# Optimization experiments

Hardware: AMD Instinct MI355X
Metric: run time of the kernel (lower is better)

## Reference

```python
import jax, jax.numpy as jnp
import numpy as np

B, N, D = 16, 1024, 768
H = 12
HD = D // H
HID = 4 * D
EPS = 1e-6


def _layernorm(x, g, b):
    mu = jnp.mean(x, axis=-1, keepdims=True)
    var = jnp.mean(jnp.square(x - mu), axis=-1, keepdims=True)
    return (x - mu) * jax.lax.rsqrt(var + EPS) * g + b


def setup_inputs() -> dict:
    key = jax.random.key(0)
    ks = jax.random.split(key, 8)
    s_d = 1.0 / np.sqrt(D)
    s_h = 1.0 / np.sqrt(HID)
    return {
        "x": jax.random.normal(ks[0], (B, N, D), dtype=jnp.float32),
        "qkv_w": jax.random.uniform(ks[1], (3 * D, D), jnp.float32, -s_d, s_d),
        "proj_w": jax.random.uniform(ks[2], (D, D), jnp.float32, -s_d, s_d),
        "proj_b": jax.random.uniform(ks[3], (D,), jnp.float32, -s_d, s_d),
        "fc1_w": jax.random.uniform(ks[4], (HID, D), jnp.float32, -s_d, s_d),
        "fc1_b": jax.random.uniform(ks[5], (HID,), jnp.float32, -s_d, s_d),
        "fc2_w": jax.random.uniform(ks[6], (D, HID), jnp.float32, -s_h, s_h),
        "fc2_b": jax.random.uniform(ks[7], (D,), jnp.float32, -s_h, s_h),
        "norm1_g": jnp.ones((D,), jnp.float32),
        "norm1_b": jnp.zeros((D,), jnp.float32),
        "norm2_g": jnp.ones((D,), jnp.float32),
        "norm2_b": jnp.zeros((D,), jnp.float32),
    }


def _attention(x, qkv_w, proj_w, proj_b):
    b, n, _ = x.shape
    qkv = x @ qkv_w.T                                  # [b,n,3D] (no bias: qkv_bias=False)
    qkv = qkv.reshape(b, n, 3, H, HD)
    q, k, v = (jnp.transpose(qkv[:, :, i], (0, 2, 1, 3)) for i in range(3))  # [b,h,n,hd]
    scale = HD ** (-0.5)
    dots = jnp.einsum("bhid,bhjd->bhij", q, k) * scale
    attn = jax.nn.softmax(dots, axis=-1)
    out = jnp.einsum("bhij,bhjd->bhid", attn, v)
    out = jnp.transpose(out, (0, 2, 1, 3)).reshape(b, n, H * HD)
    return out @ proj_w.T + proj_b


def _mlp(x, fc1_w, fc1_b, fc2_w, fc2_b):
    h = jax.nn.gelu(x @ fc1_w.T + fc1_b, approximate=False)
    return h @ fc2_w.T + fc2_b


def reference(x, qkv_w, proj_w, proj_b, fc1_w, fc1_b, fc2_w, fc2_b,
              norm1_g, norm1_b, norm2_g, norm2_b):
    x = x + _attention(_layernorm(x, norm1_g, norm1_b), qkv_w, proj_w, proj_b)
    x = x + _mlp(_layernorm(x, norm2_g, norm2_b), fc1_w, fc1_b, fc2_w, fc2_b)
    return x
```

## Files before the change

### kernel.cpp

```cpp
#include <hip/hip_runtime.h>
#include <hip/hip_bf16.h>
#include <math.h>

using bf16 = __hip_bfloat16;
typedef __attribute__((ext_vector_type(8))) short short8;
typedef __attribute__((ext_vector_type(4))) short shortx4;
typedef __attribute__((ext_vector_type(4))) float floatx4;

#define BB 16
#define NN 1024
#define DD 768
#define HH 12
#define HD 64
#define HID 3072

__device__ __forceinline__ floatx4 mfma_bf16(short8 a, short8 b, floatx4 c) {
  return __builtin_amdgcn_mfma_f32_16x16x32_bf16(a, b, c, 0, 0, 0);
}

__device__ __forceinline__ short bf16_bits(float f) {
  union { bf16 h; short s; } u;
  u.h = __float2bfloat16(f);
  return u.s;
}

__device__ __forceinline__ void async_copy16(const void* g, void* l) {
  __builtin_amdgcn_global_load_lds(
      (const __attribute__((address_space(1))) unsigned int*)g,
      (__attribute__((address_space(3))) unsigned int*)l,
      16, 0, 0);
}

__device__ __forceinline__ float gelu_f(float x) {
  const float z = x * fmaf(0.10294324f, x * x, 2.3022082f);
  const float e = exp2f(z);
  return x - x * __builtin_amdgcn_rcpf(e + 1.0f);
}

__global__ __launch_bounds__(256)
void cvt_kernel(const float* __restrict__ in, bf16* __restrict__ out, int n4)
{
  const int i = blockIdx.x * 256 + threadIdx.x;
  if (i >= n4) return;
  const float4 v = ((const float4*)in)[i];
  shortx4 o;
  o.x = bf16_bits(v.x); o.y = bf16_bits(v.y);
  o.z = bf16_bits(v.z); o.w = bf16_bits(v.w);
  ((shortx4*)out)[i] = o;
}

__global__ __launch_bounds__(256)
void ln_kernel(const float* __restrict__ x, const float* __restrict__ g,
               const float* __restrict__ b, bf16* __restrict__ y)
{
  const int row = blockIdx.x;
  const int t = threadIdx.x;
  const float* xr = x + (size_t)row * DD;
  float v[3];
  float s = 0.f, s2 = 0.f;
#pragma unroll
  for (int i = 0; i < 3; ++i) {
    float f = xr[t + i * 256];
    v[i] = f;
    s += f;
    s2 += f * f;
  }
#pragma unroll
  for (int off = 1; off < 64; off <<= 1) {
    s  += __shfl_xor(s, off);
    s2 += __shfl_xor(s2, off);
  }
  __shared__ float red[2][4];
  const int wave = t >> 6, lane = t & 63;
  if (lane == 0) { red[0][wave] = s; red[1][wave] = s2; }
  __syncthreads();
  s  = red[0][0] + red[0][1] + red[0][2] + red[0][3];
  s2 = red[1][0] + red[1][1] + red[1][2] + red[1][3];
  const float mu = s * (1.f / DD);
  const float var = s2 * (1.f / DD) - mu * mu;
  const float inv = rsqrtf(var + 1e-6f);
  bf16* yr = y + (size_t)row * DD;
#pragma unroll
  for (int i = 0; i < 3; ++i) {
    int c = t + i * 256;
    yr[c] = __float2bfloat16((v[i] - mu) * inv * g[c] + b[c]);
  }
}

template <int EPI>
__global__ __launch_bounds__(256, 4)
void gemm_kernel(const bf16* __restrict__ A, const bf16* __restrict__ W,
                 const float* __restrict__ bias, const float* __restrict__ res,
                 void* __restrict__ Cv, int N, int K)
{
  __shared__ __align__(16) short smem[16896];
  short* sA = smem;
  short* sB = smem + 8192;

  const int tid  = threadIdx.x;
  const int lane = tid & 63;
  const int wave = tid >> 6;
  const int wm = wave & 1, wn = wave >> 1;
  const int row16 = lane & 15, quad = lane >> 4;

  const int lin = blockIdx.y * gridDim.x + blockIdx.x;
  const int per = gridDim.x * 8;
  const int pan = lin / per, rem = lin % per;
  const int bm = (pan * 8 + (rem & 7)) * 128;
  const int bn = (rem >> 3) * 128;

  const int lrow = lane >> 3;
  const int lkc  = (lane & 7) ^ lrow;

  const bf16* Ag = A + (size_t)(bm + wave * 32 + lrow) * K + lkc * 8;
  const bf16* Bg = W + (size_t)(bn + wave * 32 + lrow) * K + lkc * 8;
  short* sAw = sA + wave * 2048;
  short* sBw = sB + wave * 2048;

  floatx4 acc[4][4] = {};

  for (int kt = 0; kt < K; kt += 64) {
#pragma unroll
    for (int g = 0; g < 4; ++g) {
      async_copy16(Ag + (size_t)g * 8 * K + kt, sAw + g * 512);
      async_copy16(Bg + (size_t)g * 8 * K + kt, sBw + g * 512);
    }
    __syncthreads();
#pragma unroll
    for (int c = 0; c < 2; ++c) {
      short8 af[4], bfr[4];
      const int kc = c * 4 + quad;
#pragma unroll
      for (int mt = 0; mt < 4; ++mt) {
        const int row = wm * 64 + mt * 16 + row16;
        af[mt] = *(const short8*)&sA[(row >> 3) * 512 + ((row & 7) * 8 + (kc ^ (row & 7))) * 8];
      }
#pragma unroll
      for (int nt = 0; nt < 4; ++nt) {
        const int row = wn * 64 + nt * 16 + row16;
        bfr[nt] = *(const short8*)&sB[(row >> 3) * 512 + ((row & 7) * 8 + (kc ^ (row & 7))) * 8];
      }
#pragma unroll
      for (int mt = 0; mt < 4; ++mt)
#pragma unroll
        for (int nt = 0; nt < 4; ++nt)
          acc[mt][nt] = mfma_bf16(bfr[nt], af[mt], acc[mt][nt]);
    }
    __syncthreads();
  }

  if (EPI == 1) {
#pragma unroll
    for (int mt = 0; mt < 4; ++mt) {
      const int row = bm + wm * 64 + mt * 16 + row16;
#pragma unroll
      for (int nt = 0; nt < 4; ++nt) {
        const int col = bn + wn * 64 + nt * 16 + quad * 4;
        const floatx4 bv = *(const floatx4*)&bias[col];
        const floatx4 rv = *(const floatx4*)&res[(size_t)row * N + col];
        floatx4 o;
#pragma unroll
        for (int r = 0; r < 4; ++r) o[r] = acc[mt][nt][r] + bv[r] + rv[r];
        *(floatx4*)&((float*)Cv)[(size_t)row * N + col] = o;
      }
    }
  } else {
    short* sC = smem;
#pragma unroll
    for (int mt = 0; mt < 4; ++mt) {
      const int lr = wm * 64 + mt * 16 + row16;
#pragma unroll
      for (int nt = 0; nt < 4; ++nt) {
        const int lc = wn * 64 + nt * 16 + quad * 4;
        floatx4 bv = {};
        if (EPI == 2) bv = *(const floatx4*)&bias[bn + lc];
        shortx4 pk;
#pragma unroll
        for (int r = 0; r < 4; ++r) {
          float v = acc[mt][nt][r] + bv[r];
          if (EPI == 2) v = gelu_f(v);
          pk[r] = bf16_bits(v);
        }
        *(shortx4*)&sC[lr * 132 + lc] = pk;
      }
    }
    __syncthreads();
#pragma unroll
    for (int it = 0; it < 8; ++it) {
      const int row = (tid >> 4) + it * 16;
      const int col = (tid & 15) * 8;
      short8 v = *(const short8*)&sC[row * 132 + col];
      *(short8*)&((bf16*)Cv)[(size_t)(bm + row) * N + bn + col] = v;
    }
  }
}

__global__ __launch_bounds__(256)
void vtrans_kernel(const bf16* __restrict__ qkv, bf16* __restrict__ vt)
{
  const int bh = blockIdx.y;
  const int b = bh / HH, h = bh % HH;
  const int n0 = blockIdx.x * 64;
  __shared__ __align__(16) short tile[64 * 72];
  const int tid = threadIdx.x;

  const int r = tid >> 2, c16 = (tid & 3) * 16;
  const bf16* src = qkv + (size_t)(b * NN + n0 + r) * 2304 + 2 * DD + h * 64 + c16;
  *(short8*)&tile[r * 72 + c16]     = *(const short8*)(src);
  *(short8*)&tile[r * 72 + c16 + 8] = *(const short8*)(src + 8);
  __syncthreads();

#pragma unroll
  for (int it = 0; it < 2; ++it) {
    const int d  = (tid >> 3) + it * 32;
    const int jg = (tid & 7) * 8;
    short8 o;
#pragma unroll
    for (int t = 0; t < 8; ++t) ((short*)&o)[t] = tile[(jg + t) * 72 + d];
    *(short8*)&vt[((size_t)bh * 64 + d) * NN + n0 + jg] = o;
  }
}

__global__ __launch_bounds__(256, 2)
void attn_kernel(const bf16* __restrict__ qkv, const bf16* __restrict__ vt,
                 bf16* __restrict__ out)
{
  const int bh = blockIdx.y;
  const int b = bh / HH, h = bh % HH;
  const int q0 = blockIdx.x * 128;
  const int tid = threadIdx.x;
  const int lane = tid & 63;
  const int wave = tid >> 6;
  const int row16 = lane & 15, quad = lane >> 4;

  __shared__ __align__(16) short sK[64 * 72];
  __shared__ __align__(16) short sVt[64 * 72];
  __shared__ __align__(16) short sP[4][32 * 72];

  const bf16* base  = qkv + (size_t)b * NN * 2304 + h * 64;
  const bf16* vbase = vt + (size_t)bh * 64 * NN;

  short8 qf[2][2];
#pragma unroll
  for (int qg = 0; qg < 2; ++qg) {
    const bf16* qrow = base + (size_t)(q0 + wave * 32 + qg * 16 + row16) * 2304;
    qf[qg][0] = *(const short8*)(qrow + quad * 8);
    qf[qg][1] = *(const short8*)(qrow + 32 + quad * 8);
  }

  floatx4 o_acc[2][4] = {};
  floatx4 l_acc[2] = {};
  const short8 ones = { (short)0x3F80, (short)0x3F80, (short)0x3F80, (short)0x3F80,
                        (short)0x3F80, (short)0x3F80, (short)0x3F80, (short)0x3F80 };

  const int sr = tid >> 2;
  const int sc = (tid & 3) * 16;
  const float ESC = 0.1803368801f;

  for (int jt = 0; jt < NN / 64; ++jt) {
    const int j0 = jt * 64;
    {
      const bf16* kp = base + (size_t)(j0 + sr) * 2304 + DD + sc;
      *(short8*)&sK[sr * 72 + sc]     = *(const short8*)(kp);
      *(short8*)&sK[sr * 72 + sc + 8] = *(const short8*)(kp + 8);
      const bf16* vp = vbase + (size_t)sr * NN + j0 + sc;
      *(short8*)&sVt[sr * 72 + sc]     = *(const short8*)(vp);
      *(short8*)&sVt[sr * 72 + sc + 8] = *(const short8*)(vp + 8);
    }
    __syncthreads();

#pragma unroll
    for (int nt = 0; nt < 4; ++nt) {
      short8 kb0 = *(const short8*)&sK[(nt * 16 + row16) * 72 + quad * 8];
      short8 kb1 = *(const short8*)&sK[(nt * 16 + row16) * 72 + 32 + quad * 8];
#pragma unroll
      for (int qg = 0; qg < 2; ++qg) {
        floatx4 st = {};
        st = mfma_bf16(kb0, qf[qg][0], st);
        st = mfma_bf16(kb1, qf[qg][1], st);
        shortx4 pk;
#pragma unroll
        for (int r = 0; r < 4; ++r)
          pk[r] = bf16_bits(exp2f(fminf(st[r] * ESC, 30.f)));
        *(shortx4*)&sP[wave][(qg * 16 + row16) * 72 + nt * 16 + quad * 4] = pk;
      }
    }

    short8 vb[4][2];
#pragma unroll
    for (int dt = 0; dt < 4; ++dt) {
      vb[dt][0] = *(const short8*)&sVt[(dt * 16 + row16) * 72 + quad * 8];
      vb[dt][1] = *(const short8*)&sVt[(dt * 16 + row16) * 72 + 32 + quad * 8];
    }
#pragma unroll
    for (int qg = 0; qg < 2; ++qg) {
      short8 pf0 = *(const short8*)&sP[wave][(qg * 16 + row16) * 72 + quad * 8];
      short8 pf1 = *(const short8*)&sP[wave][(qg * 16 + row16) * 72 + 32 + quad * 8];
      l_acc[qg] = mfma_bf16(pf0, ones, l_acc[qg]);
      l_acc[qg] = mfma_bf16(pf1, ones, l_acc[qg]);
#pragma unroll
      for (int dt = 0; dt < 4; ++dt) {
        o_acc[qg][dt] = mfma_bf16(pf0, vb[dt][0], o_acc[qg][dt]);
        o_acc[qg][dt] = mfma_bf16(pf1, vb[dt][1], o_acc[qg][dt]);
      }
    }
    __syncthreads();
  }

#pragma unroll
  for (int qg = 0; qg < 2; ++qg) {
#pragma unroll
    for (int r = 0; r < 4; ++r) {
      const float inv = 1.f / l_acc[qg][r];
      const size_t n = (size_t)(b * NN + q0 + wave * 32 + qg * 16 + quad * 4 + r);
#pragma unroll
      for (int dt = 0; dt < 4; ++dt) {
        out[n * DD + h * 64 + dt * 16 + row16] =
            __float2bfloat16(o_acc[qg][dt][r] * inv);
      }
    }
  }
}

extern "C" void kernel_launch(void* const* d_in, const int* in_sizes, int n_in,
                              void* d_out, int out_size, void* d_ws, size_t ws_size,
                              hipStream_t stream)
{
  const float* x       = (const float*)d_in[0];
  const float* qkv_w   = (const float*)d_in[1];
  const float* proj_w  = (const float*)d_in[2];
  const float* proj_b  = (const float*)d_in[3];
  const float* fc1_w   = (const float*)d_in[4];
  const float* fc1_b   = (const float*)d_in[5];
  const float* fc2_w   = (const float*)d_in[6];
  const float* fc2_b   = (const float*)d_in[7];
  const float* norm1_g = (const float*)d_in[8];
  const float* norm1_b = (const float*)d_in[9];
  const float* norm2_g = (const float*)d_in[10];
  const float* norm2_b = (const float*)d_in[11];
  float* out = (float*)d_out;

  const int M = BB * NN;
  char* ws = (char*)d_ws;

  bf16* wq = (bf16*)ws;
  bf16* wp = wq + (size_t)3 * DD * DD;
  bf16* w1 = wp + (size_t)DD * DD;
  bf16* w2 = w1 + (size_t)HID * DD;
  bf16* xn = w2 + (size_t)DD * HID;
  char* p2 = (char*)(xn + (size_t)M * DD);
  const size_t base_b = (size_t)(p2 - ws);

  int NBc = 1;
  for (int c = 16; c >= 1; c >>= 1)
    if (ws_size >= base_b + (size_t)c * 1024 * 7680) { NBc = c; break; }

  const int Rc = NBc * NN;
  bf16* qkvb = (bf16*)p2;
  bf16* aob  = qkvb + (size_t)Rc * 2304;
  bf16* vtb  = aob  + (size_t)Rc * DD;
  bf16* hb   = (bf16*)p2;

  cvt_kernel<<<(3 * DD * DD / 4 + 255) / 256, 256, 0, stream>>>(qkv_w, wq, 3 * DD * DD / 4);
  cvt_kernel<<<(DD * DD / 4 + 255) / 256, 256, 0, stream>>>(proj_w, wp, DD * DD / 4);
  cvt_kernel<<<(HID * DD / 4 + 255) / 256, 256, 0, stream>>>(fc1_w, w1, HID * DD / 4);
  cvt_kernel<<<(DD * HID / 4 + 255) / 256, 256, 0, stream>>>(fc2_w, w2, DD * HID / 4);

  ln_kernel<<<M, 256, 0, stream>>>(x, norm1_g, norm1_b, xn);

  for (int c = 0; c < BB / NBc; ++c) {
    const size_t r0 = (size_t)c * Rc;
    gemm_kernel<0><<<dim3(3 * DD / 128, Rc / 128), 256, 0, stream>>>(
        xn + r0 * DD, wq, nullptr, nullptr, qkvb, 3 * DD, DD);
    vtrans_kernel<<<dim3(NN / 64, NBc * HH), 256, 0, stream>>>(qkvb, vtb);
    attn_kernel<<<dim3(NN / 128, NBc * HH), 256, 0, stream>>>(qkvb, vtb, aob);
    gemm_kernel<1><<<dim3(DD / 128, Rc / 128), 256, 0, stream>>>(
        aob, wp, proj_b, x + r0 * DD, out + r0 * DD, DD, DD);
  }

  ln_kernel<<<M, 256, 0, stream>>>(out, norm2_g, norm2_b, xn);

  for (int c = 0; c < BB / NBc; ++c) {
    const size_t r0 = (size_t)c * Rc;
    gemm_kernel<2><<<dim3(HID / 128, Rc / 128), 256, 0, stream>>>(
        xn + r0 * DD, w1, fc1_b, nullptr, hb, HID, DD);
    gemm_kernel<1><<<dim3(DD / 128, Rc / 128), 256, 0, stream>>>(
        hb, w2, fc2_b, out + r0 * DD, out + r0 * DD, DD, HID);
  }
}
```

Measured before the change: 558.2 us.

## Prefetch K/V tiles asynchronously and double query rows per attention block

The attention kernel now has each wave handle 64 query rows instead of 32, so a block covers 256 queries and half as many blocks are launched. K and V tiles are loaded into shared memory in a fragment-ordered layout with async copies. The next tile's copy is issued right after the current tile's fragments are read into registers, so the global loads overlap the MFMA and exp work. The softmax probability buffer is also re-laid out so each fragment is read with one contiguous vector load. The change cuts K/V reload traffic and load latency, but it raises register pressure and gives fewer blocks for occupancy.

```diff
diff --git a/kernel.cpp b/kernel.cpp
--- a/kernel.cpp
+++ b/kernel.cpp
@@ -227,75 +227,90 @@
 {
   const int bh = blockIdx.y;
   const int b = bh / HH, h = bh % HH;
-  const int q0 = blockIdx.x * 128;
+  const int q0 = blockIdx.x * 256;
   const int tid = threadIdx.x;
   const int lane = tid & 63;
   const int wave = tid >> 6;
   const int row16 = lane & 15, quad = lane >> 4;
 
-  __shared__ __align__(16) short sK[64 * 72];
-  __shared__ __align__(16) short sVt[64 * 72];
-  __shared__ __align__(16) short sP[4][32 * 72];
+  __shared__ __align__(16) short sK[4096];
+  __shared__ __align__(16) short sVt[4096];
+  __shared__ __align__(16) short sP[4][4][1024];
 
   const bf16* base  = qkv + (size_t)b * NN * 2304 + h * 64;
   const bf16* vbase = vt + (size_t)bh * 64 * NN;
 
-  short8 qf[2][2];
-#pragma unroll
-  for (int qg = 0; qg < 2; ++qg) {
-    const bf16* qrow = base + (size_t)(q0 + wave * 32 + qg * 16 + row16) * 2304;
+  short8 qf[4][2];
+#pragma unroll
+  for (int qg = 0; qg < 4; ++qg) {
+    const bf16* qrow = base + (size_t)(q0 + wave * 64 + qg * 16 + row16) * 2304;
     qf[qg][0] = *(const short8*)(qrow + quad * 8);
     qf[qg][1] = *(const short8*)(qrow + 32 + quad * 8);
   }
 
-  floatx4 o_acc[2][4] = {};
-  floatx4 l_acc[2] = {};
+  floatx4 o_acc[4][4] = {};
+  floatx4 l_acc[4] = {};
   const short8 ones = { (short)0x3F80, (short)0x3F80, (short)0x3F80, (short)0x3F80,
                         (short)0x3F80, (short)0x3F80, (short)0x3F80, (short)0x3F80 };
 
-  const int sr = tid >> 2;
-  const int sc = (tid & 3) * 16;
+  const bf16* ksrc = base + DD + (size_t)(wave * 16 + row16) * 2304 + quad * 8;
+  const bf16* vsrc = vbase + (size_t)(wave * 16 + row16) * NN + quad * 8;
+  short* kdst = sK + wave * 1024 + lane * 8;
+  short* vdst = sVt + wave * 1024 + lane * 8;
+
+  async_copy16(ksrc, kdst);
+  async_copy16(ksrc + 32, kdst + 512);
+  async_copy16(vsrc, vdst);
+  async_copy16(vsrc + 32, vdst + 512);
+
   const float ESC = 0.1803368801f;
 
   for (int jt = 0; jt < NN / 64; ++jt) {
-    const int j0 = jt * 64;
-    {
-      const bf16* kp = base + (size_t)(j0 + sr) * 2304 + DD + sc;
-      *(short8*)&sK[sr * 72 + sc]     = *(const short8*)(kp);
-      *(short8*)&sK[sr * 72 + sc + 8] = *(const short8*)(kp + 8);
-      const bf16* vp = vbase + (size_t)sr * NN + j0 + sc;
-      *(short8*)&sVt[sr * 72 + sc]     = *(const short8*)(vp);
-      *(short8*)&sVt[sr * 72 + sc + 8] = *(const short8*)(vp + 8);
-    }
     __syncthreads();
 
+    short8 vb[4][2];
+#pragma unroll
+    for (int dt = 0; dt < 4; ++dt) {
+      vb[dt][0] = *(const short8*)&sVt[dt * 1024 + lane * 8];
+      vb[dt][1] = *(const short8*)&sVt[dt * 1024 + 512 + lane * 8];
+    }
+    short8 kb[4][2];
 #pragma unroll
     for (int nt = 0; nt < 4; ++nt) {
-      short8 kb0 = *(const short8*)&sK[(nt * 16 + row16) * 72 + quad * 8];
-      short8 kb1 = *(const short8*)&sK[(nt * 16 + row16) * 72 + 32 + quad * 8];
-#pragma unroll
-      for (int qg = 0; qg < 2; ++qg) {
+      kb[nt][0] = *(const short8*)&sK[nt * 1024 + lane * 8];
+      kb[nt][1] = *(const short8*)&sK[nt * 1024 + 512 + lane * 8];
+    }
+    __syncthreads();
+
+    if (jt + 1 < NN / 64) {
+      const bf16* k2 = ksrc + (size_t)(jt + 1) * 64 * 2304;
+      const bf16* v2 = vsrc + (jt + 1) * 64;
+      async_copy16(k2, kdst);
+      async_copy16(k2 + 32, kdst + 512);
+      async_copy16(v2, vdst);
+      async_copy16(v2 + 32, vdst + 512);
+    }
+
+#pragma unroll
+    for (int nt = 0; nt < 4; ++nt) {
+#pragma unroll
+      for (int qg = 0; qg < 4; ++qg) {
         floatx4 st = {};
-        st = mfma_bf16(kb0, qf[qg][0], st);
-        st = mfma_bf16(kb1, qf[qg][1], st);
+        st = mfma_bf16(kb[nt][0], qf[qg][0], st);
+        st = mfma_bf16(kb[nt][1], qf[qg][1], st);
         shortx4 pk;
 #pragma unroll
         for (int r = 0; r < 4; ++r)
           pk[r] = bf16_bits(exp2f(fminf(st[r] * ESC, 30.f)));
-        *(shortx4*)&sP[wave][(qg * 16 + row16) * 72 + nt * 16 + quad * 4] = pk;
-      }
-    }
-
-    short8 vb[4][2];
-#pragma unroll
-    for (int dt = 0; dt < 4; ++dt) {
-      vb[dt][0] = *(const short8*)&sVt[(dt * 16 + row16) * 72 + quad * 8];
-      vb[dt][1] = *(const short8*)&sVt[(dt * 16 + row16) * 72 + 32 + quad * 8];
-    }
-#pragma unroll
-    for (int qg = 0; qg < 2; ++qg) {
-      short8 pf0 = *(const short8*)&sP[wave][(qg * 16 + row16) * 72 + quad * 8];
-      short8 pf1 = *(const short8*)&sP[wave][(qg * 16 + row16) * 72 + 32 + quad * 8];
+        *(shortx4*)&sP[wave][qg][(row16 + 16 * (2 * nt + (quad >> 1))) * 8 +
+                                 (quad & 1) * 4] = pk;
+      }
+    }
+
+#pragma unroll
+    for (int qg = 0; qg < 4; ++qg) {
+      const short8 pf0 = *(const short8*)&sP[wave][qg][lane * 8];
+      const short8 pf1 = *(const short8*)&sP[wave][qg][512 + lane * 8];
       l_acc[qg] = mfma_bf16(pf0, ones, l_acc[qg]);
       l_acc[qg] = mfma_bf16(pf1, ones, l_acc[qg]);
 #pragma unroll
@@ -304,15 +319,14 @@
         o_acc[qg][dt] = mfma_bf16(pf1, vb[dt][1], o_acc[qg][dt]);
       }
     }
-    __syncthreads();
-  }
-
-#pragma unroll
-  for (int qg = 0; qg < 2; ++qg) {
+  }
+
+#pragma unroll
+  for (int qg = 0; qg < 4; ++qg) {
 #pragma unroll
     for (int r = 0; r < 4; ++r) {
       const float inv = 1.f / l_acc[qg][r];
-      const size_t n = (size_t)(b * NN + q0 + wave * 32 + qg * 16 + quad * 4 + r);
+      const size_t n = (size_t)(b * NN + q0 + wave * 64 + qg * 16 + quad * 4 + r);
 #pragma unroll
       for (int dt = 0; dt < 4; ++dt) {
         out[n * DD + h * 64 + dt * 16 + row16] =
@@ -373,7 +387,7 @@
     gemm_kernel<0><<<dim3(3 * DD / 128, Rc / 128), 256, 0, stream>>>(
         xn + r0 * DD, wq, nullptr, nullptr, qkvb, 3 * DD, DD);
     vtrans_kernel<<<dim3(NN / 64, NBc * HH), 256, 0, stream>>>(qkvb, vtb);
-    attn_kernel<<<dim3(NN / 128, NBc * HH), 256, 0, stream>>>(qkvb, vtb, aob);
+    attn_kernel<<<dim3(NN / 256, NBc * HH), 256, 0, stream>>>(qkvb, vtb, aob);
     gemm_kernel<1><<<dim3(DD / 128, Rc / 128), 256, 0, stream>>>(
         aob, wp, proj_b, x + r0 * DD, out + r0 * DD, DD, DD);
   }
```

After: 531.6 us. 1.05x faster.
